# Optimization experiments

Hardware: AMD Instinct MI355X
Metric: run time of the kernel (lower is better)

Reference implementation:

```python
import jax, jax.numpy as jnp
import numpy as np

EPS = 1e-6
EVAL_STEPS = 7
INV_T = 1.0
B, C, H, W = 16, 512, 64, 64
S, R = 1, 64


def setup_inputs() -> dict:
    key = jax.random.key(0)
    kx, kb = jax.random.split(key)
    x = jax.random.uniform(kx, (B, C, H, W), dtype=jnp.float32)
    # bases: F.normalize(rand(S, D, R), dim=1), repeated over batch -> [B*S, D, R]
    D = C // S
    b = jax.random.uniform(kb, (S, D, R), dtype=jnp.float32)
    b = b / jnp.clip(jnp.linalg.norm(b, axis=1, keepdims=True), 1e-12)
    bases = jnp.tile(b, (B, 1, 1))  # [B*S, D, R]
    return {"x": x, "bases": bases}


def _local_step(x, bases, coef):
    # x: [BS, D, N], bases: [BS, D, R], coef: [BS, N, R]
    numer = jnp.einsum('bdn,bdr->bnr', x, bases)
    denom = jnp.einsum('bnr,brk->bnk', coef, jnp.einsum('bdr,bdk->brk', bases, bases))
    coef = coef * numer / (denom + EPS)
    numer = jnp.einsum('bdn,bnr->bdr', x, coef)
    denom = jnp.einsum('bdr,brk->bdk', bases, jnp.einsum('bnr,bnk->brk', coef, coef))
    bases = bases * numer / (denom + EPS)
    return bases, coef


def reference(x, bases):
    batch, channels, height, width = x.shape
    scale = channels // S
    xf = x.reshape(batch * S, scale, height * width)  # [BS, D, N]
    # local_inference (eval mode: eval_steps iterations)
    coef = jnp.einsum('bdn,bdr->bnr', xf, bases)
    coef = jax.nn.softmax(INV_T * coef, axis=-1)
    for _ in range(EVAL_STEPS):
        bases, coef = _local_step(xf, bases, coef)
    # compute_coef: one extra coef update
    numer = jnp.einsum('bdn,bdr->bnr', xf, bases)
    denom = jnp.einsum('bnr,brk->bnk', coef, jnp.einsum('bdr,bdk->brk', bases, bases))
    coef = coef * numer / (denom + EPS)
    out = jnp.einsum('bdr,bnr->bdn', bases, coef)  # bases @ coef^T
    return out.reshape(batch, channels, height, width)
```

## Files before the change

### kernel.cpp

```cpp
#include <hip/hip_runtime.h>
#include <math.h>

#define EPS 1e-6f

constexpr int BSZ = 16;
constexpr int DD  = 512;
constexpr int NN  = 4096;
constexpr int RR  = 64;
constexpr int STEPS = 7;
constexpr int NS_B  = 8;
constexpr int NS_C  = 32;
constexpr int NS_N2 = 8;

typedef _Float16 half_t;
typedef __attribute__((ext_vector_type(8))) _Float16 half8;
typedef __attribute__((ext_vector_type(4))) float f32x4;

__device__ __forceinline__ void fma4s(float4& a, const float4& b, float s) {
  a.x = fmaf(b.x, s, a.x); a.y = fmaf(b.y, s, a.y);
  a.z = fmaf(b.z, s, a.z); a.w = fmaf(b.w, s, a.w);
}
__device__ __forceinline__ void add4(float4& a, const float4& b) {
  a.x += b.x; a.y += b.y; a.z += b.z; a.w += b.w;
}
__device__ __forceinline__ f32x4 mfmah(half8 a, half8 b, f32x4 c) {
  return __builtin_amdgcn_mfma_f32_16x16x32_f16(a, b, c, 0, 0, 0);
}

__device__ __forceinline__ void gload16(const float* g, float* l) {
  __builtin_amdgcn_global_load_lds(
      (const __attribute__((address_space(1))) void*)g,
      (__attribute__((address_space(3))) void*)l, 16, 0, 0);
}

__global__ void __launch_bounds__(256) tcvt16_kernel(const float* __restrict__ src,
                                                     half_t* __restrict__ dh,
                                                     int R, int C) {
  __shared__ float tileT[64 * 65];
  const int b = blockIdx.z, c0 = blockIdx.x << 6, r0 = blockIdx.y << 6;
  const float* sp = src + (long long)b * R * C;
  const int t = threadIdx.x;
  #pragma unroll
  for (int i = 0; i < 4; ++i) {
    const int idx = t + (i << 8);
    const int row = idx >> 4, c4 = (idx & 15) << 2;
    const float4 v = *(const float4*)&sp[(long long)(r0 + row) * C + c0 + c4];
    tileT[(c4 + 0) * 65 + row] = v.x;
    tileT[(c4 + 1) * 65 + row] = v.y;
    tileT[(c4 + 2) * 65 + row] = v.z;
    tileT[(c4 + 3) * 65 + row] = v.w;
  }
  __syncthreads();
  const int orow = t >> 2, och = (t & 3) << 4;
  half8 h0, h1;
  #pragma unroll
  for (int j = 0; j < 8; ++j) h0[j] = (half_t)tileT[orow * 65 + och + j];
  #pragma unroll
  for (int j = 0; j < 8; ++j) h1[j] = (half_t)tileT[orow * 65 + och + 8 + j];
  const long long ob = ((long long)b * C + c0 + orow) * R + r0 + och;
  *(half8*)&dh[ob] = h0;
  *(half8*)&dh[ob + 8] = h1;
}

__global__ void __launch_bounds__(256) cast16_kernel(const float* __restrict__ src,
                                                     half_t* __restrict__ dst,
                                                     long long n) {
  const long long i = ((long long)blockIdx.x * 256 + threadIdx.x) * 8;
  if (i >= n) return;
  const float4 a = *(const float4*)&src[i];
  const float4 c = *(const float4*)&src[i + 4];
  half8 h;
  h[0] = (half_t)a.x; h[1] = (half_t)a.y; h[2] = (half_t)a.z; h[3] = (half_t)a.w;
  h[4] = (half_t)c.x; h[5] = (half_t)c.y; h[6] = (half_t)c.z; h[7] = (half_t)c.w;
  *(half8*)&dst[i] = h;
}

__global__ void __launch_bounds__(256) btb16_kernel(const half_t* __restrict__ BT,
                                                    half_t* __restrict__ Gh) {
  __shared__ float red[64 * 64];
  const int b = blockIdx.x;
  const int t = threadIdx.x;
  const int w = t >> 6;
  const int l = t & 63;
  const int row16 = l & 15;
  const int koff  = (l >> 4) << 3;

  const half_t* ap = BT + ((long long)b * RR + row16) * DD + (w << 7) + koff;

  f32x4 acc[4][4];
  #pragma unroll
  for (int i = 0; i < 4; ++i)
    #pragma unroll
    for (int j = 0; j < 4; ++j) acc[i][j] = (f32x4){0.f, 0.f, 0.f, 0.f};

  #pragma unroll
  for (int kt = 0; kt < 4; ++kt) {
    const int ko = kt << 5;
    half8 af[4];
    #pragma unroll
    for (int rs = 0; rs < 4; ++rs) af[rs] = *(const half8*)&ap[(long long)rs * 16 * DD + ko];
    #pragma unroll
    for (int r1 = 0; r1 < 4; ++r1)
      #pragma unroll
      for (int r2 = 0; r2 < 4; ++r2)
        acc[r1][r2] = mfmah(af[r1], af[r2], acc[r1][r2]);
  }
  for (int ww = 0; ww < 4; ++ww) {
    if (w == ww) {
      #pragma unroll
      for (int r1 = 0; r1 < 4; ++r1)
        #pragma unroll
        for (int r2 = 0; r2 < 4; ++r2)
          #pragma unroll
          for (int j = 0; j < 4; ++j) {
            const int row = (r1 << 4) + ((l >> 4) << 2) + j;
            const int col = (r2 << 4) + row16;
            if (ww == 0) red[row * 64 + col] = acc[r1][r2][j];
            else         red[row * 64 + col] += acc[r1][r2][j];
          }
    }
    __syncthreads();
  }
  for (int i = t; i < 512; i += 256) {
    half8 h;
    #pragma unroll
    for (int j = 0; j < 8; ++j) h[j] = (half_t)red[(i << 3) + j];
    *(half8*)&Gh[(long long)b * 4096 + (i << 3)] = h;
  }
}

template <int MODE>
__global__ void __launch_bounds__(128) fused16_kernel(const half_t* __restrict__ xT,
                                                      const half_t* __restrict__ BT,
                                                      const half_t* __restrict__ Gh,
                                                      float* __restrict__ coef,
                                                      half_t* __restrict__ cbT,
                                                      half_t* __restrict__ cN) {
  __shared__ half_t ctile[(MODE == 1) ? 64 * 40 : 8];
  const int b  = blockIdx.y;
  const int n0 = blockIdx.x << 5;
  const int t  = threadIdx.x;
  const int w  = t >> 6;
  const int l  = t & 63;
  const int row16 = l & 15;
  const int koff  = (l >> 4) << 3;
  const int nrb   = n0 + (w << 4);

  const half_t* ap = xT + ((long long)b * NN + nrb + row16) * DD + koff;
  const half_t* bp = BT + ((long long)b * RR + row16) * DD + koff;

  f32x4 acc[4];
  #pragma unroll
  for (int rs = 0; rs < 4; ++rs) acc[rs] = (f32x4){0.f, 0.f, 0.f, 0.f};

  #pragma unroll
  for (int kt = 0; kt < 16; ++kt) {
    const int ko = kt << 5;
    const half8 av = *(const half8*)&ap[ko];
    #pragma unroll
    for (int rs = 0; rs < 4; ++rs) {
      const half8 bv = *(const half8*)&bp[rs * 16 * DD + ko];
      acc[rs] = mfmah(av, bv, acc[rs]);
    }
  }

  if constexpr (MODE == 0) {
    #pragma unroll
    for (int j = 0; j < 4; ++j) {
      float m = fmaxf(fmaxf(acc[0][j], acc[1][j]), fmaxf(acc[2][j], acc[3][j]));
      m = fmaxf(m, __shfl_xor(m, 1));
      m = fmaxf(m, __shfl_xor(m, 2));
      m = fmaxf(m, __shfl_xor(m, 4));
      m = fmaxf(m, __shfl_xor(m, 8));
      float s = 0.f;
      #pragma unroll
      for (int rs = 0; rs < 4; ++rs) { acc[rs][j] = __expf(acc[rs][j] - m); s += acc[rs][j]; }
      s += __shfl_xor(s, 1); s += __shfl_xor(s, 2);
      s += __shfl_xor(s, 4); s += __shfl_xor(s, 8);
      const float inv = 1.f / s;
      #pragma unroll
      for (int rs = 0; rs < 4; ++rs) acc[rs][j] *= inv;
    }
    #pragma unroll
    for (int rs = 0; rs < 4; ++rs)
      #pragma unroll
      for (int j = 0; j < 4; ++j)
        coef[((long long)b * NN + nrb + ((l >> 4) << 2) + j) * RR + (rs << 4) + row16] = acc[rs][j];
  } else {
    const float* crow = coef + ((long long)b * NN + nrb + row16) * RR;
    const half_t* ghb = Gh + (long long)b * 4096;
    f32x4 dn[4];
    #pragma unroll
    for (int rs = 0; rs < 4; ++rs) dn[rs] = (f32x4){0.f, 0.f, 0.f, 0.f};
    #pragma unroll
    for (int kt = 0; kt < 2; ++kt) {
      const int ko = (kt << 5) + koff;
      const float4 c0 = *(const float4*)&crow[ko];
      const float4 c1 = *(const float4*)&crow[ko + 4];
      half8 ch;
      ch[0] = (half_t)c0.x; ch[1] = (half_t)c0.y; ch[2] = (half_t)c0.z; ch[3] = (half_t)c0.w;
      ch[4] = (half_t)c1.x; ch[5] = (half_t)c1.y; ch[6] = (half_t)c1.z; ch[7] = (half_t)c1.w;
      #pragma unroll
      for (int rs = 0; rs < 4; ++rs) {
        const half8 gh = *(const half8*)&ghb[((rs << 4) + row16) * 64 + ko];
        dn[rs] = mfmah(ch, gh, dn[rs]);
      }
    }
    #pragma unroll
    for (int rs = 0; rs < 4; ++rs)
      #pragma unroll
      for (int j = 0; j < 4; ++j) {
        const int r = (rs << 4) + row16;
        const int nl = ((w << 4) + ((l >> 4) << 2) + j);
        const long long idx = ((long long)b * NN + n0 + nl) * RR + r;
        const float co = coef[idx];
        const float v  = co * acc[rs][j] / (dn[rs][j] + EPS);
        if constexpr (MODE == 1) {
          coef[idx] = v;
          ctile[r * 40 + nl] = (half_t)v;
        } else {
          cN[idx] = (half_t)v;
        }
      }
    if constexpr (MODE == 1) {
      __syncthreads();
      if (t < 64) {
        half_t* dst = cbT + ((long long)b * RR + t) * NN + n0;
        *(half8*)&dst[0]  = *(const half8*)&ctile[t * 40 + 0];
        *(half8*)&dst[8]  = *(const half8*)&ctile[t * 40 + 8];
        *(half8*)&dst[16] = *(const half8*)&ctile[t * 40 + 16];
        *(half8*)&dst[24] = *(const half8*)&ctile[t * 40 + 24];
      }
    }
  }
}

__global__ void __launch_bounds__(256) ctc16_kernel(const half_t* __restrict__ cbT,
                                                    float* __restrict__ ctcp) {
  const int b  = blockIdx.y;
  const int t  = threadIdx.x;
  const int w  = t >> 6;
  const int l  = t & 63;
  const int row16 = l & 15;
  const int koff  = (l >> 4) << 3;
  const int sp2   = blockIdx.x * 4 + w;
  const int nbeg  = sp2 * 128;

  const half_t* ap = cbT + ((long long)b * RR + row16) * NN + nbeg + koff;

  f32x4 acc[4][4];
  #pragma unroll
  for (int i = 0; i < 4; ++i)
    #pragma unroll
    for (int j = 0; j < 4; ++j) acc[i][j] = (f32x4){0.f, 0.f, 0.f, 0.f};

  #pragma unroll
  for (int kt = 0; kt < 4; ++kt) {
    const int ko = kt << 5;
    half8 af[4];
    #pragma unroll
    for (int rs = 0; rs < 4; ++rs) af[rs] = *(const half8*)&ap[(long long)rs * 16 * NN + ko];
    #pragma unroll
    for (int r1 = 0; r1 < 4; ++r1)
      #pragma unroll
      for (int r2 = 0; r2 < 4; ++r2)
        acc[r1][r2] = mfmah(af[r1], af[r2], acc[r1][r2]);
  }
  float* op = ctcp + ((long long)sp2 * BSZ + b) * 4096;
  #pragma unroll
  for (int r1 = 0; r1 < 4; ++r1)
    #pragma unroll
    for (int r2 = 0; r2 < 4; ++r2)
      #pragma unroll
      for (int j = 0; j < 4; ++j)
        op[((r1 << 4) + ((l >> 4) << 2) + j) * 64 + (r2 << 4) + row16] = acc[r1][r2][j];
}

__global__ void __launch_bounds__(128) numer2_16_kernel(const half_t* __restrict__ xh,
                                                        const half_t* __restrict__ cbT,
                                                        float* __restrict__ n2p) {
  const int b  = blockIdx.z;
  const int s  = blockIdx.y;
  const int d0 = blockIdx.x << 6;
  const int t  = threadIdx.x;
  const int w  = t >> 6;
  const int l  = t & 63;
  const int row16 = l & 15;
  const int koff  = (l >> 4) << 3;
  const int nbeg  = s * (NN / NS_N2);

  const half_t* ap = xh + ((long long)b * DD + d0 + w * 32 + row16) * NN + nbeg + koff;
  const half_t* cp = cbT + ((long long)b * RR + row16) * NN + nbeg + koff;

  f32x4 acc[2][4];
  #pragma unroll
  for (int ds = 0; ds < 2; ++ds)
    #pragma unroll
    for (int rs = 0; rs < 4; ++rs) acc[ds][rs] = (f32x4){0.f, 0.f, 0.f, 0.f};

  #pragma unroll
  for (int kt = 0; kt < 16; ++kt) {
    const int ko = kt << 5;
    half8 av[2], bf[4];
    #pragma unroll
    for (int ds = 0; ds < 2; ++ds) av[ds] = *(const half8*)&ap[(long long)ds * 16 * NN + ko];
    #pragma unroll
    for (int rs = 0; rs < 4; ++rs) bf[rs] = *(const half8*)&cp[(long long)rs * 16 * NN + ko];
    #pragma unroll
    for (int ds = 0; ds < 2; ++ds)
      #pragma unroll
      for (int rs = 0; rs < 4; ++rs)
        acc[ds][rs] = mfmah(av[ds], bf[rs], acc[ds][rs]);
  }
  float* op = n2p + (((long long)s * BSZ + b) * DD + d0 + w * 32) * RR;
  #pragma unroll
  for (int ds = 0; ds < 2; ++ds)
    #pragma unroll
    for (int rs = 0; rs < 4; ++rs)
      #pragma unroll
      for (int j = 0; j < 4; ++j)
        op[(long long)(ds * 16 + ((l >> 4) << 2) + j) * RR + (rs << 4) + row16] = acc[ds][rs][j];
}

__global__ void __launch_bounds__(256) out16_kernel(const half_t* __restrict__ bD,
                                                    const half_t* __restrict__ cN,
                                                    float* __restrict__ out) {
  __shared__ float ot[16 * 264];
  const int n0 = blockIdx.x << 8;
  const int d0 = blockIdx.y << 4;
  const int b  = blockIdx.z;
  const int t  = threadIdx.x;
  const int w  = t >> 6;
  const int l  = t & 63;
  const int row16 = l & 15;
  const int koff  = (l >> 4) << 3;

  const half_t* ap = bD + ((long long)b * DD + d0 + row16) * RR + koff;
  const half_t* bp = cN + ((long long)b * NN + n0 + (w << 6) + row16) * RR + koff;

  f32x4 acc[4];
  #pragma unroll
  for (int ns = 0; ns < 4; ++ns) acc[ns] = (f32x4){0.f, 0.f, 0.f, 0.f};

  #pragma unroll
  for (int kt = 0; kt < 2; ++kt) {
    const int ko = kt << 5;
    const half8 av = *(const half8*)&ap[ko];
    #pragma unroll
    for (int ns = 0; ns < 4; ++ns) {
      const half8 bv = *(const half8*)&bp[(long long)ns * 16 * RR + ko];
      acc[ns] = mfmah(av, bv, acc[ns]);
    }
  }
  #pragma unroll
  for (int ns = 0; ns < 4; ++ns)
    #pragma unroll
    for (int j = 0; j < 4; ++j)
      ot[(((l >> 4) << 2) + j) * 264 + (w << 6) + (ns << 4) + row16] = acc[ns][j];
  __syncthreads();
  #pragma unroll
  for (int k = 0; k < 4; ++k) {
    const int idx = t + (k << 8);
    const int row = idx >> 6, c4 = (idx & 63) << 2;
    const float4 v = *(const float4*)&ot[row * 264 + c4];
    *(float4*)&out[((long long)b * DD + d0 + row) * NN + n0 + c4] = v;
  }
}

__global__ void __launch_bounds__(256) bupdate_fb_kernel(float* __restrict__ Bw,
                                                         const float* __restrict__ n2p,
                                                         const float* __restrict__ ctcp,
                                                         int ns2) {
  __shared__ float ct[4096];
  const int b  = blockIdx.y;
  const int d0 = blockIdx.x << 6;
  #pragma unroll
  for (int i = 0; i < 4; ++i) {
    const int w = threadIdx.x + (i << 8);
    float4 s = make_float4(0.f, 0.f, 0.f, 0.f);
    for (int sp = 0; sp < NS_C; ++sp)
      add4(s, ((const float4*)(ctcp + ((long long)sp * BSZ + b) * 4096))[w]);
    ((float4*)ct)[w] = s;
  }
  __syncthreads();
  const int d  = d0 + (threadIdx.x >> 2);
  const int rq = (threadIdx.x & 3) << 4;

  float4 ns[4];
  #pragma unroll
  for (int j = 0; j < 4; ++j) ns[j] = make_float4(0.f, 0.f, 0.f, 0.f);
  for (int s = 0; s < ns2; ++s) {
    const float4* p = (const float4*)&n2p[(((long long)s * BSZ + b) * DD + d) * RR + rq];
    #pragma unroll
    for (int j = 0; j < 4; ++j) add4(ns[j], p[j]);
  }
  const float4* brow = (const float4*)&Bw[((long long)b * DD + d) * RR];
  float4 dn[4];
  #pragma unroll
  for (int j = 0; j < 4; ++j) dn[j] = make_float4(0.f, 0.f, 0.f, 0.f);
  for (int q = 0; q < 16; ++q) {
    const float4 b4 = brow[q];
    const float4* c0 = (const float4*)&ct[(4 * q + 0) * 64 + rq];
    const float4* c1 = (const float4*)&ct[(4 * q + 1) * 64 + rq];
    const float4* c2 = (const float4*)&ct[(4 * q + 2) * 64 + rq];
    const float4* c3 = (const float4*)&ct[(4 * q + 3) * 64 + rq];
    #pragma unroll
    for (int j = 0; j < 4; ++j) {
      fma4s(dn[j], c0[j], b4.x); fma4s(dn[j], c1[j], b4.y);
      fma4s(dn[j], c2[j], b4.z); fma4s(dn[j], c3[j], b4.w);
    }
  }
  float4* bp = (float4*)&Bw[((long long)b * DD + d) * RR + rq];
  float4 bo[4];
  #pragma unroll
  for (int j = 0; j < 4; ++j) bo[j] = bp[j];
  __syncthreads();
  #pragma unroll
  for (int j = 0; j < 4; ++j) {
    float4 o;
    o.x = bo[j].x * ns[j].x / (dn[j].x + EPS);
    o.y = bo[j].y * ns[j].y / (dn[j].y + EPS);
    o.z = bo[j].z * ns[j].z / (dn[j].z + EPS);
    o.w = bo[j].w * ns[j].w / (dn[j].w + EPS);
    bp[j] = o;
  }
}

__global__ void __launch_bounds__(256) gram_kernel(const float* __restrict__ M,
                                                   float* __restrict__ outp,
                                                   int rowsPerWave,
                                                   long long batchStride) {
  __shared__ float red[RR * RR];
  const int lane = threadIdx.x & 63;
  const int wid  = threadIdx.x >> 6;
  const int b    = blockIdx.y;
  const long long rowbase = (long long)(blockIdx.x * 4 + wid) * rowsPerWave;
  const float* Mp = M + (long long)b * batchStride + rowbase * RR;
  float acc[RR];
  #pragma unroll
  for (int k = 0; k < RR; ++k) acc[k] = 0.f;
  #pragma unroll 2
  for (int rr = 0; rr < rowsPerWave; ++rr) {
    const float v = Mp[(long long)rr * RR + lane];
    #pragma unroll
    for (int k = 0; k < RR; ++k) acc[k] = fmaf(__shfl(v, k), v, acc[k]);
  }
  for (int w = 0; w < 4; ++w) {
    if (wid == w) {
      if (w == 0) {
        #pragma unroll
        for (int k = 0; k < RR; ++k) red[k * RR + lane] = acc[k];
      } else {
        #pragma unroll
        for (int k = 0; k < RR; ++k) red[k * RR + lane] += acc[k];
      }
    }
    __syncthreads();
  }
  float* op = outp + ((long long)blockIdx.x * BSZ + b) * (RR * RR);
  for (int i = threadIdx.x; i < RR * RR; i += 256) op[i] = red[i];
}


template <int MODE>
__global__ void __launch_bounds__(128) fused_coef_kernel(const float* __restrict__ X,
                                                         const float* __restrict__ Bw,
                                                         const float* __restrict__ btbp,
                                                         float* __restrict__ coef) {
  __shared__ float lds[8192];
  const int b    = blockIdx.y;
  const int n0   = blockIdx.x << 6;
  const int t    = threadIdx.x;
  const int wid  = t >> 6;
  const int lane = t & 63;
  const int rgrp = t & 7;
  const int ngrp = t >> 3;
  const int nl   = ngrp << 2;
  const int r0   = rgrp << 3;
  const float* Xp = X  + (long long)b * DD * NN + n0;
  const float* Bp = Bw + (long long)b * DD * RR;

  float4 acc[4][2];
  #pragma unroll
  for (int i = 0; i < 4; ++i) { acc[i][0] = make_float4(0,0,0,0); acc[i][1] = make_float4(0,0,0,0); }

  auto stage = [&](int buf, int d0) {
    float* xd = lds + (buf << 11);
    float* bd = lds + 4096 + (buf << 11);
    const int rsub = lane >> 4;
    const int c4   = (lane & 15) << 2;
    #pragma unroll
    for (int j = 0; j < 4; ++j) {
      const int q   = (wid << 2) + j;
      const int row = (q << 2) + rsub;
      gload16(&Xp[(long long)(d0 + row) * NN + c4], xd + (q << 8));
      gload16(&Bp[(long long)(d0 + row) * RR + c4], bd + (q << 8));
    }
  };

  stage(0, 0);
  __syncthreads();
  for (int kt = 0; kt < 16; ++kt) {
    const int cur = kt & 1;
    if (kt + 1 < 16) stage(cur ^ 1, (kt + 1) << 5);
    const float* xs = lds + (cur << 11);
    const float* bs = lds + 4096 + (cur << 11);
    #pragma unroll 8
    for (int dd = 0; dd < 32; ++dd) {
      const float4 xv  = *(const float4*)&xs[(dd << 6) + nl];
      const float4 bv0 = *(const float4*)&bs[(dd << 6) + r0];
      const float4 bv1 = *(const float4*)&bs[(dd << 6) + r0 + 4];
      fma4s(acc[0][0], bv0, xv.x); fma4s(acc[0][1], bv1, xv.x);
      fma4s(acc[1][0], bv0, xv.y); fma4s(acc[1][1], bv1, xv.y);
      fma4s(acc[2][0], bv0, xv.z); fma4s(acc[2][1], bv1, xv.z);
      fma4s(acc[3][0], bv0, xv.w); fma4s(acc[3][1], bv1, xv.w);
    }
    __syncthreads();
  }

  if constexpr (MODE == 0) {
    #pragma unroll
    for (int i = 0; i < 4; ++i) {
      float4 a0 = acc[i][0], a1 = acc[i][1];
      float m = fmaxf(fmaxf(fmaxf(a0.x, a0.y), fmaxf(a0.z, a0.w)),
                      fmaxf(fmaxf(a1.x, a1.y), fmaxf(a1.z, a1.w)));
      m = fmaxf(m, __shfl_xor(m, 1));
      m = fmaxf(m, __shfl_xor(m, 2));
      m = fmaxf(m, __shfl_xor(m, 4));
      a0.x = __expf(a0.x - m); a0.y = __expf(a0.y - m);
      a0.z = __expf(a0.z - m); a0.w = __expf(a0.w - m);
      a1.x = __expf(a1.x - m); a1.y = __expf(a1.y - m);
      a1.z = __expf(a1.z - m); a1.w = __expf(a1.w - m);
      float s = a0.x + a0.y + a0.z + a0.w + a1.x + a1.y + a1.z + a1.w;
      s += __shfl_xor(s, 1); s += __shfl_xor(s, 2); s += __shfl_xor(s, 4);
      const float inv = 1.f / s;
      a0.x *= inv; a0.y *= inv; a0.z *= inv; a0.w *= inv;
      a1.x *= inv; a1.y *= inv; a1.z *= inv; a1.w *= inv;
      float* cp = coef + ((long long)b * NN + n0 + nl + i) * RR + r0;
      *(float4*)&cp[0] = a0;
      *(float4*)&cp[4] = a1;
    }
  } else {
    float4* G4  = (float4*)lds;
    float4* CO4 = (float4*)(lds + 4096);
    #pragma unroll
    for (int j = 0; j < 8; ++j) {
      const int wi = t + (j << 7);
      float4 ssum = make_float4(0,0,0,0);
      #pragma unroll
      for (int sp = 0; sp < NS_B; ++sp)
        add4(ssum, ((const float4*)(btbp + ((long long)sp * BSZ + b) * 4096))[wi]);
      G4[wi] = ssum;
    }
    const float4* cof4 = (const float4*)(coef + ((long long)b * NN + n0) * RR);
    #pragma unroll
    for (int j = 0; j < 8; ++j) {
      const int wi = t + (j << 7);
      const int row = wi >> 4, c4 = wi & 15;
      CO4[(row << 4) + (c4 ^ ((row >> 2) & 7))] = cof4[wi];
    }
    __syncthreads();
    const int g = ngrp & 7;
    float4 dn[4][2];
    #pragma unroll
    for (int i = 0; i < 4; ++i) { dn[i][0] = make_float4(0,0,0,0); dn[i][1] = make_float4(0,0,0,0); }
    #pragma unroll 4
    for (int kq = 0; kq < 16; ++kq) {
      float4 g0[4], g1[4];
      #pragma unroll
      for (int jj = 0; jj < 4; ++jj) {
        g0[jj] = G4[(((kq << 2) + jj) << 4) + (rgrp << 1)];
        g1[jj] = G4[(((kq << 2) + jj) << 4) + (rgrp << 1) + 1];
      }
      #pragma unroll
      for (int i = 0; i < 4; ++i) {
        const float4 cv = CO4[((nl + i) << 4) + (kq ^ g)];
        fma4s(dn[i][0], g0[0], cv.x); fma4s(dn[i][1], g1[0], cv.x);
        fma4s(dn[i][0], g0[1], cv.y); fma4s(dn[i][1], g1[1], cv.y);
        fma4s(dn[i][0], g0[2], cv.z); fma4s(dn[i][1], g1[2], cv.z);
        fma4s(dn[i][0], g0[3], cv.w); fma4s(dn[i][1], g1[3], cv.w);
      }
    }
    #pragma unroll
    for (int i = 0; i < 4; ++i) {
      const int row = nl + i;
      const float4 c0 = CO4[(row << 4) + ((rgrp << 1) ^ g)];
      const float4 c1 = CO4[(row << 4) + (((rgrp << 1) + 1) ^ g)];
      float4 o0, o1;
      o0.x = c0.x * acc[i][0].x / (dn[i][0].x + EPS);
      o0.y = c0.y * acc[i][0].y / (dn[i][0].y + EPS);
      o0.z = c0.z * acc[i][0].z / (dn[i][0].z + EPS);
      o0.w = c0.w * acc[i][0].w / (dn[i][0].w + EPS);
      o1.x = c1.x * acc[i][1].x / (dn[i][1].x + EPS);
      o1.y = c1.y * acc[i][1].y / (dn[i][1].y + EPS);
      o1.z = c1.z * acc[i][1].z / (dn[i][1].z + EPS);
      o1.w = c1.w * acc[i][1].w / (dn[i][1].w + EPS);
      float* cp = coef + ((long long)b * NN + n0 + row) * RR + r0;
      *(float4*)&cp[0] = o0;
      *(float4*)&cp[4] = o1;
    }
  }
}

__global__ void __launch_bounds__(128) numer2_kernel(const float* __restrict__ X,
                                                     const float* __restrict__ coef,
                                                     float* __restrict__ n2p) {
  __shared__ float lds[8192];
  const int b    = blockIdx.z;
  const int s    = blockIdx.y;
  const int d0   = blockIdx.x << 6;
  const int t    = threadIdx.x;
  const int wid  = t >> 6;
  const int lane = t & 63;
  const int rgrp = t & 7;
  const int dgrp = t >> 3;
  const int dl   = dgrp << 2;
  const int r0   = rgrp << 3;
  const int nbeg = s * (NN / NS_N2);
  const float* Xp = X + (long long)b * DD * NN + (long long)d0 * NN;
  const float* Cp = coef + (long long)b * NN * RR;

  float4 acc[4][2];
  #pragma unroll
  for (int i = 0; i < 4; ++i) { acc[i][0] = make_float4(0,0,0,0); acc[i][1] = make_float4(0,0,0,0); }

  auto stage = [&](int buf, int nb) {
    float* xd = lds + (buf << 11);
    float* cd = lds + 4096 + (buf << 11);
    {
      const int rsub = lane >> 3, c4 = lane & 7;
      #pragma unroll
      for (int j = 0; j < 4; ++j) {
        const int q   = (wid << 2) + j;
        const int row = (q << 3) + rsub;
        const int sc  = (c4 ^ ((row >> 2) & 7)) << 2;
        gload16(&Xp[(long long)row * NN + nb + sc], xd + (q << 8));
      }
    }
    {
      const int rsub = lane >> 4, c4 = (lane & 15) << 2;
      #pragma unroll
      for (int j = 0; j < 4; ++j) {
        const int q   = (wid << 2) + j;
        const int row = (q << 2) + rsub;
        gload16(&Cp[(long long)(nb + row) * RR + c4], cd + (q << 8));
      }
    }
  };

  stage(0, nbeg);
  __syncthreads();
  const int g = dgrp & 7;
  for (int kt = 0; kt < (NN / NS_N2) / 32; ++kt) {
    const int cur = kt & 1;
    if (kt + 1 < (NN / NS_N2) / 32) stage(cur ^ 1, nbeg + ((kt + 1) << 5));
    const float* xs = lds + (cur << 11);
    const float* cs = lds + 4096 + (cur << 11);
    #pragma unroll 8
    for (int nn = 0; nn < 32; ++nn) {
      const int col = ((((nn >> 2) ^ g) << 2) + (nn & 3));
      float xe[4];
      #pragma unroll
      for (int i = 0; i < 4; ++i) xe[i] = xs[((dl + i) << 5) + col];
      const float4 cv0 = *(const float4*)&cs[(nn << 6) + r0];
      const float4 cv1 = *(const float4*)&cs[(nn << 6) + r0 + 4];
      #pragma unroll
      for (int i = 0; i < 4; ++i) {
        fma4s(acc[i][0], cv0, xe[i]);
        fma4s(acc[i][1], cv1, xe[i]);
      }
    }
    __syncthreads();
  }
  #pragma unroll
  for (int i = 0; i < 4; ++i) {
    float* op = n2p + (((long long)s * BSZ + b) * DD + d0 + dl + i) * RR + r0;
    *(float4*)&op[0] = acc[i][0];
    *(float4*)&op[4] = acc[i][1];
  }
}

__global__ void __launch_bounds__(256) out_kernel(const float* __restrict__ Bw,
                                                  const float* __restrict__ coef,
                                                  float* __restrict__ out) {
  __shared__ float bt [64 * 68];
  __shared__ float ctl[64 * 68];
  const int n0 = blockIdx.x << 6;
  const int d0 = blockIdx.y << 6;
  const int b  = blockIdx.z;
  const int tx = threadIdx.x & 15;
  const int ty = threadIdx.x >> 4;
  for (int t = threadIdx.x; t < 1024; t += 256) {
    const int row = t >> 4, c4 = (t & 15) << 2;
    const float4 v = *(const float4*)&Bw[((long long)b * DD + d0 + row) * RR + c4];
    bt[(c4 + 0) * 68 + row] = v.x; bt[(c4 + 1) * 68 + row] = v.y;
    bt[(c4 + 2) * 68 + row] = v.z; bt[(c4 + 3) * 68 + row] = v.w;
  }
  for (int t = threadIdx.x; t < 1024; t += 256) {
    const int row = t >> 4, c4 = (t & 15) << 2;
    const float4 v = *(const float4*)&coef[((long long)b * NN + n0 + row) * RR + c4];
    ctl[(c4 + 0) * 68 + row] = v.x; ctl[(c4 + 1) * 68 + row] = v.y;
    ctl[(c4 + 2) * 68 + row] = v.z; ctl[(c4 + 3) * 68 + row] = v.w;
  }
  __syncthreads();
  float4 ai[4];
  #pragma unroll
  for (int i = 0; i < 4; ++i) ai[i] = make_float4(0.f, 0.f, 0.f, 0.f);
  #pragma unroll 8
  for (int r = 0; r < 64; ++r) {
    const float4 bv = *(const float4*)&bt [r * 68 + (ty << 2)];
    const float4 cv = *(const float4*)&ctl[r * 68 + (tx << 2)];
    fma4s(ai[0], cv, bv.x); fma4s(ai[1], cv, bv.y);
    fma4s(ai[2], cv, bv.z); fma4s(ai[3], cv, bv.w);
  }
  #pragma unroll
  for (int i = 0; i < 4; ++i)
    *(float4*)&out[((long long)b * DD + d0 + (ty << 2) + i) * NN + n0 + (tx << 2)] = ai[i];
}

extern "C" void kernel_launch(void* const* d_in, const int* in_sizes, int n_in,
                              void* d_out, int out_size, void* d_ws, size_t ws_size,
                              hipStream_t stream) {
  const float* x        = (const float*)d_in[0];
  const float* bases_in = (const float*)d_in[1];
  float* out = (float*)d_out;
  float* ws  = (float*)d_ws;

  float* coef    = ws;
  float* bases_w = coef + (long long)BSZ * NN * RR;
  float* btbp    = bases_w + (long long)BSZ * DD * RR;
  float* ctcp    = btbp + (long long)NS_B * BSZ * 4096;
  float* n2p     = ctcp + (long long)NS_C * BSZ * 4096;
  float* ctcs    = n2p + (long long)NS_N2 * BSZ * DD * RR;
  half_t* xT16   = (half_t*)(ctcs + (long long)BSZ * 4096);
  half_t* xd16   = xT16 + (long long)BSZ * NN * DD;
  half_t* BbT16  = xd16 + (long long)BSZ * NN * DD;
  half_t* cbT16  = BbT16 + (long long)BSZ * RR * DD;
  half_t* Gh16   = cbT16 + (long long)BSZ * RR * NN;
  const long long need = (long long)((char*)(Gh16 + (long long)BSZ * 4096) - (char*)d_ws);

  half_t* cN16 = (half_t*)n2p;
  half_t* bD16 = cN16 + (long long)BSZ * NN * RR;

  const dim3 blk256(256);
  const dim3 blk128(128);

  hipMemcpyAsync(bases_w, bases_in, sizeof(float) * BSZ * DD * RR,
                 hipMemcpyDeviceToDevice, stream);

  if ((long long)ws_size >= need) {
    cast16_kernel<<<dim3(16384), blk256, 0, stream>>>(x, xd16, (long long)BSZ * DD * NN);
    tcvt16_kernel<<<dim3(NN / 64, DD / 64, BSZ), blk256, 0, stream>>>(x, xT16, DD, NN);
    tcvt16_kernel<<<dim3(1, DD / 64, BSZ), blk256, 0, stream>>>(bases_w, BbT16, DD, RR);
    fused16_kernel<0><<<dim3(NN / 32, BSZ), blk128, 0, stream>>>(
        xT16, BbT16, nullptr, coef, nullptr, nullptr);

    for (int it = 0; it < STEPS; ++it) {
      tcvt16_kernel<<<dim3(1, DD / 64, BSZ), blk256, 0, stream>>>(bases_w, BbT16, DD, RR);
      btb16_kernel<<<dim3(BSZ), blk256, 0, stream>>>(BbT16, Gh16);
      fused16_kernel<1><<<dim3(NN / 32, BSZ), blk128, 0, stream>>>(
          xT16, BbT16, Gh16, coef, cbT16, nullptr);
      ctc16_kernel<<<dim3(8, BSZ), blk256, 0, stream>>>(cbT16, ctcp);
      numer2_16_kernel<<<dim3(DD / 64, NS_N2, BSZ), blk128, 0, stream>>>(xd16, cbT16, n2p);
      bupdate_fb_kernel<<<dim3(DD / 64, BSZ), blk256, 0, stream>>>(bases_w, n2p, ctcp, NS_N2);
    }
    tcvt16_kernel<<<dim3(1, DD / 64, BSZ), blk256, 0, stream>>>(bases_w, BbT16, DD, RR);
    btb16_kernel<<<dim3(BSZ), blk256, 0, stream>>>(BbT16, Gh16);
    fused16_kernel<2><<<dim3(NN / 32, BSZ), blk128, 0, stream>>>(
        xT16, BbT16, Gh16, coef, nullptr, cN16);
    cast16_kernel<<<dim3(256), blk256, 0, stream>>>(bases_w, bD16, (long long)BSZ * DD * RR);
    out16_kernel<<<dim3(NN / 256, DD / 16, BSZ), blk256, 0, stream>>>(bD16, cN16, out);
  } else {
    fused_coef_kernel<0><<<dim3(NN / 64, BSZ), blk128, 0, stream>>>(x, bases_w, nullptr, coef);
    for (int it = 0; it < STEPS; ++it) {
      gram_kernel<<<dim3(NS_B, BSZ), blk256, 0, stream>>>(bases_w, btbp, DD / (NS_B * 4),
                                                          (long long)DD * RR);
      fused_coef_kernel<1><<<dim3(NN / 64, BSZ), blk128, 0, stream>>>(x, bases_w, btbp, coef);
      gram_kernel<<<dim3(NS_C, BSZ), blk256, 0, stream>>>(coef, ctcp, NN / (NS_C * 4),
                                                          (long long)NN * RR);
      numer2_kernel<<<dim3(DD / 64, NS_N2, BSZ), blk128, 0, stream>>>(x, coef, n2p);
      bupdate_fb_kernel<<<dim3(DD / 64, BSZ), blk256, 0, stream>>>(bases_w, n2p, ctcp, NS_N2);
    }
    gram_kernel<<<dim3(NS_B, BSZ), blk256, 0, stream>>>(bases_w, btbp, DD / (NS_B * 4),
                                                        (long long)DD * RR);
    fused_coef_kernel<1><<<dim3(NN / 64, BSZ), blk128, 0, stream>>>(x, bases_w, btbp, coef);
    out_kernel<<<dim3(NN / 64, DD / 64, BSZ), blk256, 0, stream>>>(bases_w, coef, out);
  }
}
```

Before: 997.2 us.

## Fuse coef Gram into numer2 kernel and fold bases transpose/cast into update

The coef^T·coef Gram computation moves into the numer2 kernel as an extra block column, so one kernel launch per step replaces two and the Gram partials drop from 32 splits to 8. The bases update kernel now also writes the transposed fp16 bases and, on the last step, the fp16 row-major copy. This removes the per-step tcvt16 launch and the final cast16 launch. bD16 is relocated to the btbp region so it does not overlap cN16 in n2p.

```diff
diff --git a/kernel.cpp b/kernel.cpp
--- a/kernel.cpp
+++ b/kernel.cpp
@@ -235,60 +235,65 @@
   }
 }
 
-__global__ void __launch_bounds__(256) ctc16_kernel(const half_t* __restrict__ cbT,
-                                                    float* __restrict__ ctcp) {
-  const int b  = blockIdx.y;
-  const int t  = threadIdx.x;
-  const int w  = t >> 6;
-  const int l  = t & 63;
-  const int row16 = l & 15;
-  const int koff  = (l >> 4) << 3;
-  const int sp2   = blockIdx.x * 4 + w;
-  const int nbeg  = sp2 * 128;
-
-  const half_t* ap = cbT + ((long long)b * RR + row16) * NN + nbeg + koff;
-
-  f32x4 acc[4][4];
-  #pragma unroll
-  for (int i = 0; i < 4; ++i)
-    #pragma unroll
-    for (int j = 0; j < 4; ++j) acc[i][j] = (f32x4){0.f, 0.f, 0.f, 0.f};
-
-  #pragma unroll
-  for (int kt = 0; kt < 4; ++kt) {
-    const int ko = kt << 5;
-    half8 af[4];
-    #pragma unroll
-    for (int rs = 0; rs < 4; ++rs) af[rs] = *(const half8*)&ap[(long long)rs * 16 * NN + ko];
-    #pragma unroll
-    for (int r1 = 0; r1 < 4; ++r1)
-      #pragma unroll
-      for (int r2 = 0; r2 < 4; ++r2)
-        acc[r1][r2] = mfmah(af[r1], af[r2], acc[r1][r2]);
-  }
-  float* op = ctcp + ((long long)sp2 * BSZ + b) * 4096;
-  #pragma unroll
-  for (int r1 = 0; r1 < 4; ++r1)
-    #pragma unroll
-    for (int r2 = 0; r2 < 4; ++r2)
-      #pragma unroll
-      for (int j = 0; j < 4; ++j)
-        op[((r1 << 4) + ((l >> 4) << 2) + j) * 64 + (r2 << 4) + row16] = acc[r1][r2][j];
-}
-
-__global__ void __launch_bounds__(128) numer2_16_kernel(const half_t* __restrict__ xh,
-                                                        const half_t* __restrict__ cbT,
-                                                        float* __restrict__ n2p) {
-  const int b  = blockIdx.z;
-  const int s  = blockIdx.y;
-  const int d0 = blockIdx.x << 6;
-  const int t  = threadIdx.x;
-  const int w  = t >> 6;
-  const int l  = t & 63;
+__global__ void __launch_bounds__(128) numer2ctc16_kernel(const half_t* __restrict__ xh,
+                                                          const half_t* __restrict__ cbT,
+                                                          float* __restrict__ n2p,
+                                                          float* __restrict__ ctcp) {
+  __shared__ float red[4096];
+  const int b = blockIdx.z;
+  const int s = blockIdx.y;
+  const int t = threadIdx.x;
+  const int w = t >> 6;
+  const int l = t & 63;
   const int row16 = l & 15;
   const int koff  = (l >> 4) << 3;
   const int nbeg  = s * (NN / NS_N2);
 
+  if (blockIdx.x == DD / 64) {
+    const half_t* ap = cbT + ((long long)b * RR + row16) * NN + nbeg + (w << 8) + koff;
+    f32x4 acc[4][4];
+    #pragma unroll
+    for (int i = 0; i < 4; ++i)
+      #pragma unroll
+      for (int j = 0; j < 4; ++j) acc[i][j] = (f32x4){0.f, 0.f, 0.f, 0.f};
+    #pragma unroll
+    for (int kt = 0; kt < 8; ++kt) {
+      const int ko = kt << 5;
+      half8 af[4];
+      #pragma unroll
+      for (int rs = 0; rs < 4; ++rs) af[rs] = *(const half8*)&ap[(long long)rs * 16 * NN + ko];
+      #pragma unroll
+      for (int r1 = 0; r1 < 4; ++r1)
+        #pragma unroll
+        for (int r2 = 0; r2 < 4; ++r2)
+          acc[r1][r2] = mfmah(af[r1], af[r2], acc[r1][r2]);
+    }
+    if (w == 0) {
+      #pragma unroll
+      for (int r1 = 0; r1 < 4; ++r1)
+        #pragma unroll
+        for (int r2 = 0; r2 < 4; ++r2)
+          #pragma unroll
+          for (int j = 0; j < 4; ++j)
+            red[((r1 << 4) + ((l >> 4) << 2) + j) * 64 + (r2 << 4) + row16] = acc[r1][r2][j];
+    }
+    __syncthreads();
+    if (w == 1) {
+      #pragma unroll
+      for (int r1 = 0; r1 < 4; ++r1)
+        #pragma unroll
+        for (int r2 = 0; r2 < 4; ++r2)
+          #pragma unroll
+          for (int j = 0; j < 4; ++j)
+            red[((r1 << 4) + ((l >> 4) << 2) + j) * 64 + (r2 << 4) + row16] += acc[r1][r2][j];
+    }
+    __syncthreads();
+    float* op = ctcp + ((long long)s * BSZ + b) * 4096;
+    for (int i = t; i < 1024; i += 128) ((float4*)op)[i] = ((const float4*)red)[i];
+    return;
+  }
+
+  const int d0 = blockIdx.x << 6;
   const half_t* ap = xh + ((long long)b * DD + d0 + w * 32 + row16) * NN + nbeg + koff;
   const half_t* cp = cbT + ((long long)b * RR + row16) * NN + nbeg + koff;
 
@@ -320,6 +325,93 @@
       #pragma unroll
       for (int j = 0; j < 4; ++j)
         op[(long long)(ds * 16 + ((l >> 4) << 2) + j) * RR + (rs << 4) + row16] = acc[ds][rs][j];
+}
+
+__global__ void __launch_bounds__(256) bupdate16_kernel(float* __restrict__ Bw,
+                                                        const float* __restrict__ n2p,
+                                                        const float* __restrict__ ctcp,
+                                                        half_t* __restrict__ BbT,
+                                                        half_t* __restrict__ bD) {
+  __shared__ float ct[4096];
+  const int b  = blockIdx.y;
+  const int d0 = blockIdx.x << 6;
+  const int t  = threadIdx.x;
+  #pragma unroll
+  for (int i = 0; i < 4; ++i) {
+    const int w = t + (i << 8);
+    float4 s4 = make_float4(0.f, 0.f, 0.f, 0.f);
+    #pragma unroll
+    for (int sp = 0; sp < NS_N2; ++sp)
+      add4(s4, ((const float4*)(ctcp + ((long long)sp * BSZ + b) * 4096))[w]);
+    ((float4*)ct)[w] = s4;
+  }
+  __syncthreads();
+  const int dl = t >> 2;
+  const int d  = d0 + dl;
+  const int rq = (t & 3) << 4;
+
+  float4 ns[4];
+  #pragma unroll
+  for (int j = 0; j < 4; ++j) ns[j] = make_float4(0.f, 0.f, 0.f, 0.f);
+  for (int s = 0; s < NS_N2; ++s) {
+    const float4* p = (const float4*)&n2p[(((long long)s * BSZ + b) * DD + d) * RR + rq];
+    #pragma unroll
+    for (int j = 0; j < 4; ++j) add4(ns[j], p[j]);
+  }
+  const float4* brow = (const float4*)&Bw[((long long)b * DD + d) * RR];
+  float4 dn[4];
+  #pragma unroll
+  for (int j = 0; j < 4; ++j) dn[j] = make_float4(0.f, 0.f, 0.f, 0.f);
+  for (int q = 0; q < 16; ++q) {
+    const float4 b4 = brow[q];
+    const float4* c0 = (const float4*)&ct[(4 * q + 0) * 64 + rq];
+    const float4* c1 = (const float4*)&ct[(4 * q + 1) * 64 + rq];
+    const float4* c2 = (const float4*)&ct[(4 * q + 2) * 64 + rq];
+    const float4* c3 = (const float4*)&ct[(4 * q + 3) * 64 + rq];
+    #pragma unroll
+    for (int j = 0; j < 4; ++j) {
+      fma4s(dn[j], c0[j], b4.x); fma4s(dn[j], c1[j], b4.y);
+      fma4s(dn[j], c2[j], b4.z); fma4s(dn[j], c3[j], b4.w);
+    }
+  }
+  float4* bp = (float4*)&Bw[((long long)b * DD + d) * RR + rq];
+  float4 bo[4];
+  #pragma unroll
+  for (int j = 0; j < 4; ++j) bo[j] = bp[j];
+  __syncthreads();
+  half_t* tile = (half_t*)ct;
+  float4 ov[4];
+  #pragma unroll
+  for (int j = 0; j < 4; ++j) {
+    ov[j].x = bo[j].x * ns[j].x / (dn[j].x + EPS);
+    ov[j].y = bo[j].y * ns[j].y / (dn[j].y + EPS);
+    ov[j].z = bo[j].z * ns[j].z / (dn[j].z + EPS);
+    ov[j].w = bo[j].w * ns[j].w / (dn[j].w + EPS);
+    bp[j] = ov[j];
+    tile[(rq + (j << 2) + 0) * 64 + dl] = (half_t)ov[j].x;
+    tile[(rq + (j << 2) + 1) * 64 + dl] = (half_t)ov[j].y;
+    tile[(rq + (j << 2) + 2) * 64 + dl] = (half_t)ov[j].z;
+    tile[(rq + (j << 2) + 3) * 64 + dl] = (half_t)ov[j].w;
+  }
+  if (bD) {
+    half_t* dst = bD + ((long long)b * DD + d) * RR + rq;
+    half8 h0, h1;
+    #pragma unroll
+    for (int e = 0; e < 4; ++e) {
+      h0[e] = (half_t)ov[0].x, h0[e] = h0[e];
+    }
+    h0[0] = (half_t)ov[0].x; h0[1] = (half_t)ov[0].y; h0[2] = (half_t)ov[0].z; h0[3] = (half_t)ov[0].w;
+    h0[4] = (half_t)ov[1].x; h0[5] = (half_t)ov[1].y; h0[6] = (half_t)ov[1].z; h0[7] = (half_t)ov[1].w;
+    h1[0] = (half_t)ov[2].x; h1[1] = (half_t)ov[2].y; h1[2] = (half_t)ov[2].z; h1[3] = (half_t)ov[2].w;
+    h1[4] = (half_t)ov[3].x; h1[5] = (half_t)ov[3].y; h1[6] = (half_t)ov[3].z; h1[7] = (half_t)ov[3].w;
+    *(half8*)&dst[0] = h0;
+    *(half8*)&dst[8] = h1;
+  }
+  __syncthreads();
+  const int r = t >> 2, qc = t & 3;
+  half_t* dstT = BbT + ((long long)b * RR + r) * DD + d0 + (qc << 4);
+  *(half8*)&dstT[0] = *(const half8*)&tile[r * 64 + (qc << 4)];
+  *(half8*)&dstT[8] = *(const half8*)&tile[r * 64 + (qc << 4) + 8];
 }
 
 __global__ void __launch_bounds__(256) out16_kernel(const half_t* __restrict__ bD,
@@ -367,64 +459,6 @@
   }
 }
 
-__global__ void __launch_bounds__(256) bupdate_fb_kernel(float* __restrict__ Bw,
-                                                         const float* __restrict__ n2p,
-                                                         const float* __restrict__ ctcp,
-                                                         int ns2) {
-  __shared__ float ct[4096];
-  const int b  = blockIdx.y;
-  const int d0 = blockIdx.x << 6;
-  #pragma unroll
-  for (int i = 0; i < 4; ++i) {
-    const int w = threadIdx.x + (i << 8);
-    float4 s = make_float4(0.f, 0.f, 0.f, 0.f);
-    for (int sp = 0; sp < NS_C; ++sp)
-      add4(s, ((const float4*)(ctcp + ((long long)sp * BSZ + b) * 4096))[w]);
-    ((float4*)ct)[w] = s;
-  }
-  __syncthreads();
-  const int d  = d0 + (threadIdx.x >> 2);
-  const int rq = (threadIdx.x & 3) << 4;
-
-  float4 ns[4];
-  #pragma unroll
-  for (int j = 0; j < 4; ++j) ns[j] = make_float4(0.f, 0.f, 0.f, 0.f);
-  for (int s = 0; s < ns2; ++s) {
-    const float4* p = (const float4*)&n2p[(((long long)s * BSZ + b) * DD + d) * RR + rq];
-    #pragma unroll
-    for (int j = 0; j < 4; ++j) add4(ns[j], p[j]);
-  }
-  const float4* brow = (const float4*)&Bw[((long long)b * DD + d) * RR];
-  float4 dn[4];
-  #pragma unroll
-  for (int j = 0; j < 4; ++j) dn[j] = make_float4(0.f, 0.f, 0.f, 0.f);
-  for (int q = 0; q < 16; ++q) {
-    const float4 b4 = brow[q];
-    const float4* c0 = (const float4*)&ct[(4 * q + 0) * 64 + rq];
-    const float4* c1 = (const float4*)&ct[(4 * q + 1) * 64 + rq];
-    const float4* c2 = (const float4*)&ct[(4 * q + 2) * 64 + rq];
-    const float4* c3 = (const float4*)&ct[(4 * q + 3) * 64 + rq];
-    #pragma unroll
-    for (int j = 0; j < 4; ++j) {
-      fma4s(dn[j], c0[j], b4.x); fma4s(dn[j], c1[j], b4.y);
-      fma4s(dn[j], c2[j], b4.z); fma4s(dn[j], c3[j], b4.w);
-    }
-  }
-  float4* bp = (float4*)&Bw[((long long)b * DD + d) * RR + rq];
-  float4 bo[4];
-  #pragma unroll
-  for (int j = 0; j < 4; ++j) bo[j] = bp[j];
-  __syncthreads();
-  #pragma unroll
-  for (int j = 0; j < 4; ++j) {
-    float4 o;
-    o.x = bo[j].x * ns[j].x / (dn[j].x + EPS);
-    o.y = bo[j].y * ns[j].y / (dn[j].y + EPS);
-    o.z = bo[j].z * ns[j].z / (dn[j].z + EPS);
-    o.w = bo[j].w * ns[j].w / (dn[j].w + EPS);
-    bp[j] = o;
-  }
-}
 
 __global__ void __launch_bounds__(256) gram_kernel(const float* __restrict__ M,
                                                    float* __restrict__ outp,
@@ -460,7 +494,6 @@
   float* op = outp + ((long long)blockIdx.x * BSZ + b) * (RR * RR);
   for (int i = threadIdx.x; i < RR * RR; i += 256) op[i] = red[i];
 }
-
 
 template <int MODE>
 __global__ void __launch_bounds__(128) fused_coef_kernel(const float* __restrict__ X,
@@ -680,6 +713,65 @@
   }
 }
 
+__global__ void __launch_bounds__(256) bupdate_fb_kernel(float* __restrict__ Bw,
+                                                         const float* __restrict__ n2p,
+                                                         const float* __restrict__ ctcp,
+                                                         int ns2) {
+  __shared__ float ct[4096];
+  const int b  = blockIdx.y;
+  const int d0 = blockIdx.x << 6;
+  #pragma unroll
+  for (int i = 0; i < 4; ++i) {
+    const int w = threadIdx.x + (i << 8);
+    float4 s = make_float4(0.f, 0.f, 0.f, 0.f);
+    for (int sp = 0; sp < NS_C; ++sp)
+      add4(s, ((const float4*)(ctcp + ((long long)sp * BSZ + b) * 4096))[w]);
+    ((float4*)ct)[w] = s;
+  }
+  __syncthreads();
+  const int d  = d0 + (threadIdx.x >> 2);
+  const int rq = (threadIdx.x & 3) << 4;
+
+  float4 ns[4];
+  #pragma unroll
+  for (int j = 0; j < 4; ++j) ns[j] = make_float4(0.f, 0.f, 0.f, 0.f);
+  for (int s = 0; s < ns2; ++s) {
+    const float4* p = (const float4*)&n2p[(((long long)s * BSZ + b) * DD + d) * RR + rq];
+    #pragma unroll
+    for (int j = 0; j < 4; ++j) add4(ns[j], p[j]);
+  }
+  const float4* brow = (const float4*)&Bw[((long long)b * DD + d) * RR];
+  float4 dn[4];
+  #pragma unroll
+  for (int j = 0; j < 4; ++j) dn[j] = make_float4(0.f, 0.f, 0.f, 0.f);
+  for (int q = 0; q < 16; ++q) {
+    const float4 b4 = brow[q];
+    const float4* c0 = (const float4*)&ct[(4 * q + 0) * 64 + rq];
+    const float4* c1 = (const float4*)&ct[(4 * q + 1) * 64 + rq];
+    const float4* c2 = (const float4*)&ct[(4 * q + 2) * 64 + rq];
+    const float4* c3 = (const float4*)&ct[(4 * q + 3) * 64 + rq];
+    #pragma unroll
+    for (int j = 0; j < 4; ++j) {
+      fma4s(dn[j], c0[j], b4.x); fma4s(dn[j], c1[j], b4.y);
+      fma4s(dn[j], c2[j], b4.z); fma4s(dn[j], c3[j], b4.w);
+    }
+  }
+  float4* bp = (float4*)&Bw[((long long)b * DD + d) * RR + rq];
+  float4 bo[4];
+  #pragma unroll
+  for (int j = 0; j < 4; ++j) bo[j] = bp[j];
+  __syncthreads();
+  #pragma unroll
+  for (int j = 0; j < 4; ++j) {
+    float4 o;
+    o.x = bo[j].x * ns[j].x / (dn[j].x + EPS);
+    o.y = bo[j].y * ns[j].y / (dn[j].y + EPS);
+    o.z = bo[j].z * ns[j].z / (dn[j].z + EPS);
+    o.w = bo[j].w * ns[j].w / (dn[j].w + EPS);
+    bp[j] = o;
+  }
+}
+
 __global__ void __launch_bounds__(256) out_kernel(const float* __restrict__ Bw,
                                                   const float* __restrict__ coef,
                                                   float* __restrict__ out) {
@@ -740,7 +832,7 @@
   const long long need = (long long)((char*)(Gh16 + (long long)BSZ * 4096) - (char*)d_ws);
 
   half_t* cN16 = (half_t*)n2p;
-  half_t* bD16 = cN16 + (long long)BSZ * NN * RR;
+  half_t* bD16 = (half_t*)btbp;
 
   const dim3 blk256(256);
   const dim3 blk128(128);
@@ -756,19 +848,17 @@
         xT16, BbT16, nullptr, coef, nullptr, nullptr);
 
     for (int it = 0; it < STEPS; ++it) {
-      tcvt16_kernel<<<dim3(1, DD / 64, BSZ), blk256, 0, stream>>>(bases_w, BbT16, DD, RR);
       btb16_kernel<<<dim3(BSZ), blk256, 0, stream>>>(BbT16, Gh16);
       fused16_kernel<1><<<dim3(NN / 32, BSZ), blk128, 0, stream>>>(
           xT16, BbT16, Gh16, coef, cbT16, nullptr);
-      ctc16_kernel<<<dim3(8, BSZ), blk256, 0, stream>>>(cbT16, ctcp);
-      numer2_16_kernel<<<dim3(DD / 64, NS_N2, BSZ), blk128, 0, stream>>>(xd16, cbT16, n2p);
-      bupdate_fb_kernel<<<dim3(DD / 64, BSZ), blk256, 0, stream>>>(bases_w, n2p, ctcp, NS_N2);
-    }
-    tcvt16_kernel<<<dim3(1, DD / 64, BSZ), blk256, 0, stream>>>(bases_w, BbT16, DD, RR);
+      numer2ctc16_kernel<<<dim3(DD / 64 + 1, NS_N2, BSZ), blk128, 0, stream>>>(
+          xd16, cbT16, n2p, ctcp);
+      bupdate16_kernel<<<dim3(DD / 64, BSZ), blk256, 0, stream>>>(
+          bases_w, n2p, ctcp, BbT16, (it == STEPS - 1) ? bD16 : nullptr);
+    }
     btb16_kernel<<<dim3(BSZ), blk256, 0, stream>>>(BbT16, Gh16);
     fused16_kernel<2><<<dim3(NN / 32, BSZ), blk128, 0, stream>>>(
         xT16, BbT16, Gh16, coef, nullptr, cN16);
-    cast16_kernel<<<dim3(256), blk256, 0, stream>>>(bases_w, bD16, (long long)BSZ * DD * RR);
     out16_kernel<<<dim3(NN / 256, DD / 16, BSZ), blk256, 0, stream>>>(bD16, cN16, out);
   } else {
     fused_coef_kernel<0><<<dim3(NN / 64, BSZ), blk128, 0, stream>>>(x, bases_w, nullptr, coef);
```

Measured after the change: 923.5 us. -7.4%, faster.
